# Kernel tuning notes

Hardware: AMD Instinct MI355X
Metric: run time of the kernel (lower is better)

The kernel has to match this reference:

```python
import jax, jax.numpy as jnp
import numpy as np

DT = 0.1  # fixed RK4 step size from the constructor

def setup_inputs() -> dict:
    key = jax.random.key(0)
    k1, k2, k3 = jax.random.split(key, 3)
    B, U, H = 65536, 128, 512
    x0 = jax.random.normal(k1, (B, U), dtype=jnp.float32)
    # small init so 20 unrolled RK4 steps stay numerically tame
    W1 = jax.random.normal(k2, (U, H), dtype=jnp.float32) * (0.5 / np.sqrt(U))
    b1 = jnp.zeros((H,), dtype=jnp.float32)
    W2 = jax.random.normal(k3, (H, U), dtype=jnp.float32) * (0.5 / np.sqrt(H))
    b2 = jnp.zeros((U,), dtype=jnp.float32)
    return {"x0": x0, "W1": W1, "b1": b1, "W2": W2, "b2": b2}

def _mlp(x, W1, b1, W2, b2):
    # vector field: Dense(512, relu) -> Dense(128); time-independent
    return jnp.maximum(x @ W1 + b1, 0.0) @ W2 + b2

def _rk4_integrate(x, n_steps, W1, b1, W2, b2):
    def step(x, _):
        k1 = _mlp(x, W1, b1, W2, b2)
        k2 = _mlp(x + 0.5 * DT * k1, W1, b1, W2, b2)
        k3 = _mlp(x + 0.5 * DT * k2, W1, b1, W2, b2)
        k4 = _mlp(x + DT * k3, W1, b1, W2, b2)
        return x + (DT / 6.0) * (k1 + 2.0 * k2 + 2.0 * k3 + k4), None
    x, _ = jax.lax.scan(step, x, None, length=n_steps)
    return x

def reference(x0, W1, b1, W2, b2):
    # phase 1: integrate t in [0, t1/2 = 1.0] -> 10 RK4 steps at dt=0.1
    x = _rk4_integrate(x0, 10, W1, b1, W2, b2)
    # phase 2: n=5 macro-steps of length (1.0 - 0.0)/5 = 0.2 -> 2 RK4 steps each
    def macro(x, _):
        x = _rk4_integrate(x, 2, W1, b1, W2, b2)
        return x, None
    x, _ = jax.lax.scan(macro, x, None, length=5)
    return x
```

## Files before the change

kernel.cpp:

```cpp
#include <hip/hip_runtime.h>
#include <stdint.h>


typedef _Float16 half8 __attribute__((ext_vector_type(8)));
typedef float f32x4 __attribute__((ext_vector_type(4)));
typedef __attribute__((address_space(3))) char lchar;
typedef __attribute__((address_space(1))) char gchar;

#define KSTR 136

static __device__ __forceinline__ void gload_lds16(const void* g, void* l) {
  __builtin_amdgcn_global_load_lds((const gchar*)g, (lchar*)l, 16, 0, 0);
}

static __device__ __forceinline__ unsigned short f2h(float x) {
  union { _Float16 h; unsigned short u; } cv;
  cv.h = (_Float16)x;
  return cv.u;
}

__global__ void pack_w(const float* __restrict__ W1, const float* __restrict__ W2,
                       unsigned short* __restrict__ w1p, unsigned short* __restrict__ w2p) {
  int id = blockIdx.x * 256 + threadIdx.x;
  int lane = id & 63, fid = (id >> 6) & 127;
  int g = lane >> 4, lm = lane & 15;
  if (id < 8192) {
    int c = fid >> 4, nt = (fid >> 2) & 3, ks = fid & 3;
    int n = c * 64 + nt * 16 + lm;
#pragma unroll
    for (int j = 0; j < 8; ++j) {
      int k = ks * 32 + g * 8 + j;
      w1p[fid * 512 + lane * 8 + j] = f2h(W1[k * 512 + n]);
    }
  } else {
    int c = fid >> 4, nt = (fid >> 1) & 7, ks = fid & 1;
    int u = nt * 16 + lm;
#pragma unroll
    for (int j = 0; j < 8; ++j) {
      int k = c * 64 + ks * 32 + g * 8 + j;
      w2p[fid * 512 + lane * 8 + j] = f2h(W2[k * 128 + u]);
    }
  }
}

__global__ __launch_bounds__(512, 2) void node_rk4(
    const float* __restrict__ x0, const float* __restrict__ b1,
    const float* __restrict__ b2, const unsigned short* __restrict__ w1p,
    const unsigned short* __restrict__ w2p, float* __restrict__ out) {
  __shared__ char Wbuf[2][32768];
  __shared__ unsigned short stg[8][32][KSTR];
  __shared__ float b1s[512];
  __shared__ float b2s[128];

  const int tid = threadIdx.x;
  const int w = tid >> 6, lane = tid & 63;
  const int g = lane >> 4, lm = lane & 15;
  unsigned short(*stage)[KSTR] = stg[w];

  b1s[tid] = b1[tid];
  if (tid < 128) b2s[tid] = b2[tid];

  const int rbase = blockIdx.x * 256 + w * 32;
  f32x4 xb[2][8], xa[2][8];
#pragma unroll
  for (int mt = 0; mt < 2; ++mt)
#pragma unroll
    for (int t = 0; t < 8; ++t) {
#pragma unroll
      for (int j = 0; j < 4; ++j)
        xb[mt][t][j] = x0[(rbase + mt * 16 + g * 4 + j) * 128 + t * 16 + lm];
      xa[mt][t] = xb[mt][t];
#pragma unroll
      for (int j = 0; j < 4; ++j)
        stage[mt * 16 + g * 4 + j][t * 16 + lm] = f2h(xb[mt][t][j]);
    }

  {
    const char* s1 = (const char*)w1p;
    const char* s2 = (const char*)w2p;
#pragma unroll
    for (int q = 0; q < 2; ++q) {
      int seg = w * 2 + q;
      gload_lds16(s1 + seg * 1024 + lane * 16, Wbuf[0] + seg * 1024);
      gload_lds16(s2 + seg * 1024 + lane * 16, Wbuf[0] + 16384 + seg * 1024);
    }
  }
  __syncthreads();

#pragma unroll 1
  for (int it = 0; it < 80; ++it) {
    const int s = it & 3;
    const float wgt = (s == 0 || s == 3) ? (0.1f / 6.0f) : (0.1f / 3.0f);
    const float alph = (s < 2) ? 0.05f : 0.1f;

    half8 A1[2][4];
#pragma unroll
    for (int mt = 0; mt < 2; ++mt)
#pragma unroll
      for (int ks = 0; ks < 4; ++ks)
        A1[mt][ks] = *(const half8*)&stage[mt * 16 + lm][ks * 32 + g * 8];

    f32x4 yacc[2][8];
#pragma unroll
    for (int mt = 0; mt < 2; ++mt)
#pragma unroll
      for (int t = 0; t < 8; ++t) yacc[mt][t] = f32x4{0.f, 0.f, 0.f, 0.f};

#pragma unroll
    for (int c = 0; c < 8; ++c) {
      {
        const int cn = (c + 1) & 7;
        char* buf = Wbuf[(c + 1) & 1];
        const char* s1 = (const char*)w1p + cn * 16384;
        const char* s2 = (const char*)w2p + cn * 16384;
#pragma unroll
        for (int q = 0; q < 2; ++q) {
          int seg = w * 2 + q;
          gload_lds16(s1 + seg * 1024 + lane * 16, buf + seg * 1024);
          gload_lds16(s2 + seg * 1024 + lane * 16, buf + 16384 + seg * 1024);
        }
      }
      const char* Wb = Wbuf[c & 1];

#pragma unroll
      for (int nt = 0; nt < 4; ++nt) {
        f32x4 h0 = {0.f, 0.f, 0.f, 0.f}, h1 = {0.f, 0.f, 0.f, 0.f};
#pragma unroll
        for (int ks = 0; ks < 4; ++ks) {
          half8 bf = *(const half8*)(Wb + (nt * 4 + ks) * 1024 + lane * 16);
          h0 = __builtin_amdgcn_mfma_f32_16x16x32_f16(A1[0][ks], bf, h0, 0, 0, 0);
          h1 = __builtin_amdgcn_mfma_f32_16x16x32_f16(A1[1][ks], bf, h1, 0, 0, 0);
        }
        float bb = b1s[c * 64 + nt * 16 + lm];
#pragma unroll
        for (int j = 0; j < 4; ++j) {
          stage[g * 4 + j][nt * 16 + lm] = f2h(fmaxf(h0[j] + bb, 0.f));
          stage[16 + g * 4 + j][nt * 16 + lm] = f2h(fmaxf(h1[j] + bb, 0.f));
        }
      }

      half8 A2[2][2];
#pragma unroll
      for (int mt = 0; mt < 2; ++mt)
#pragma unroll
        for (int k2 = 0; k2 < 2; ++k2)
          A2[mt][k2] = *(const half8*)&stage[mt * 16 + lm][k2 * 32 + g * 8];

#pragma unroll
      for (int nt = 0; nt < 8; ++nt)
#pragma unroll
        for (int k2 = 0; k2 < 2; ++k2) {
          half8 bf = *(const half8*)(Wb + 16384 + (nt * 2 + k2) * 1024 + lane * 16);
          yacc[0][nt] =
              __builtin_amdgcn_mfma_f32_16x16x32_f16(A2[0][k2], bf, yacc[0][nt], 0, 0, 0);
          yacc[1][nt] =
              __builtin_amdgcn_mfma_f32_16x16x32_f16(A2[1][k2], bf, yacc[1][nt], 0, 0, 0);
        }
      __syncthreads();
    }

#pragma unroll
    for (int mt = 0; mt < 2; ++mt)
#pragma unroll
      for (int t = 0; t < 8; ++t) {
        f32x4 k = yacc[mt][t];
        float bb = b2s[t * 16 + lm];
#pragma unroll
        for (int j = 0; j < 4; ++j) k[j] += bb;
        xa[mt][t] += wgt * k;
        f32x4 xi;
        if (s == 3) {
          xb[mt][t] = xa[mt][t];
          xi = xa[mt][t];
        } else {
          xi = xb[mt][t] + alph * k;
        }
#pragma unroll
        for (int j = 0; j < 4; ++j)
          stage[mt * 16 + g * 4 + j][t * 16 + lm] = f2h(xi[j]);
      }
  }

#pragma unroll
  for (int mt = 0; mt < 2; ++mt)
#pragma unroll
    for (int t = 0; t < 8; ++t)
#pragma unroll
      for (int j = 0; j < 4; ++j)
        out[(rbase + mt * 16 + g * 4 + j) * 128 + t * 16 + lm] = xb[mt][t][j];
}

extern "C" void kernel_launch(void* const* d_in, const int* in_sizes, int n_in,
                              void* d_out, int out_size, void* d_ws, size_t ws_size,
                              hipStream_t stream) {
  const float* x0 = (const float*)d_in[0];
  const float* W1 = (const float*)d_in[1];
  const float* b1 = (const float*)d_in[2];
  const float* W2 = (const float*)d_in[3];
  const float* b2 = (const float*)d_in[4];
  float* out = (float*)d_out;

  unsigned short* w1p = (unsigned short*)d_ws;
  unsigned short* w2p = w1p + 65536;

  pack_w<<<64, 256, 0, stream>>>(W1, W2, w1p, w2p);
  node_rk4<<<256, 512, 0, stream>>>(x0, b1, b2, w1p, w2p, out);
}
```

Baseline: 2.168 ms.

## Halve block size, interleave W1/W2 chunks, store RK4 base state in fp16

Blocks shrink from 512 to 256 threads (4 waves, 128 rows) and the grid doubles to 512. The hidden dimension is now streamed in 16 chunks of 32 columns, with W1 and W2 slices packed into a single interleaved 16KB buffer, which halves LDS use per block. The fp32 RK4 base state xb is replaced by an fp16 copy to free registers, with the aim of fitting more blocks per CU. The cost is twice as many per-chunk barriers and extra rounding of the intermediate stage inputs.

```diff
diff --git a/kernel.cpp b/kernel.cpp
--- a/kernel.cpp
+++ b/kernel.cpp
@@ -18,37 +18,43 @@
   cv.h = (_Float16)x;
   return cv.u;
 }
+static __device__ __forceinline__ float h2f(unsigned short u) {
+  union { unsigned short u; _Float16 h; } cv;
+  cv.u = u;
+  return (float)cv.h;
+}
 
 __global__ void pack_w(const float* __restrict__ W1, const float* __restrict__ W2,
-                       unsigned short* __restrict__ w1p, unsigned short* __restrict__ w2p) {
+                       unsigned short* __restrict__ wp) {
   int id = blockIdx.x * 256 + threadIdx.x;
-  int lane = id & 63, fid = (id >> 6) & 127;
+  int lane = id & 63, fid = (id >> 6) & 255;
   int g = lane >> 4, lm = lane & 15;
-  if (id < 8192) {
-    int c = fid >> 4, nt = (fid >> 2) & 3, ks = fid & 3;
-    int n = c * 64 + nt * 16 + lm;
+  int c = fid >> 4, f = fid & 15;
+  if (f < 8) {
+    int nt = f >> 2, ks = f & 3;
+    int n = c * 32 + nt * 16 + lm;
 #pragma unroll
     for (int j = 0; j < 8; ++j) {
       int k = ks * 32 + g * 8 + j;
-      w1p[fid * 512 + lane * 8 + j] = f2h(W1[k * 512 + n]);
+      wp[fid * 512 + lane * 8 + j] = f2h(W1[k * 512 + n]);
     }
   } else {
-    int c = fid >> 4, nt = (fid >> 1) & 7, ks = fid & 1;
+    int nt = f - 8;
     int u = nt * 16 + lm;
 #pragma unroll
     for (int j = 0; j < 8; ++j) {
-      int k = c * 64 + ks * 32 + g * 8 + j;
-      w2p[fid * 512 + lane * 8 + j] = f2h(W2[k * 128 + u]);
+      int k = c * 32 + g * 8 + j;
+      wp[fid * 512 + lane * 8 + j] = f2h(W2[k * 128 + u]);
     }
   }
 }
 
-__global__ __launch_bounds__(512, 2) void node_rk4(
+__global__ __launch_bounds__(256, 2) void node_rk4(
     const float* __restrict__ x0, const float* __restrict__ b1,
-    const float* __restrict__ b2, const unsigned short* __restrict__ w1p,
-    const unsigned short* __restrict__ w2p, float* __restrict__ out) {
-  __shared__ char Wbuf[2][32768];
-  __shared__ unsigned short stg[8][32][KSTR];
+    const float* __restrict__ b2, const unsigned short* __restrict__ wp,
+    float* __restrict__ out) {
+  __shared__ char Wbuf[2][16384];
+  __shared__ unsigned short stg[4][32][KSTR];
   __shared__ float b1s[512];
   __shared__ float b2s[128];
 
@@ -58,32 +64,33 @@
   unsigned short(*stage)[KSTR] = stg[w];
 
   b1s[tid] = b1[tid];
+  b1s[tid + 256] = b1[tid + 256];
   if (tid < 128) b2s[tid] = b2[tid];
 
-  const int rbase = blockIdx.x * 256 + w * 32;
-  f32x4 xb[2][8], xa[2][8];
+  const int rbase = blockIdx.x * 128 + w * 32;
+  f32x4 xa[2][8];
+  ushort4 xbh[2][8];
 #pragma unroll
   for (int mt = 0; mt < 2; ++mt)
 #pragma unroll
     for (int t = 0; t < 8; ++t) {
+      f32x4 v;
 #pragma unroll
       for (int j = 0; j < 4; ++j)
-        xb[mt][t][j] = x0[(rbase + mt * 16 + g * 4 + j) * 128 + t * 16 + lm];
-      xa[mt][t] = xb[mt][t];
+        v[j] = x0[(rbase + mt * 16 + g * 4 + j) * 128 + t * 16 + lm];
+      xa[mt][t] = v;
+      ushort4 hq;
+      hq.x = f2h(v[0]); hq.y = f2h(v[1]); hq.z = f2h(v[2]); hq.w = f2h(v[3]);
+      xbh[mt][t] = hq;
 #pragma unroll
       for (int j = 0; j < 4; ++j)
-        stage[mt * 16 + g * 4 + j][t * 16 + lm] = f2h(xb[mt][t][j]);
-    }
-
-  {
-    const char* s1 = (const char*)w1p;
-    const char* s2 = (const char*)w2p;
-#pragma unroll
-    for (int q = 0; q < 2; ++q) {
-      int seg = w * 2 + q;
-      gload_lds16(s1 + seg * 1024 + lane * 16, Wbuf[0] + seg * 1024);
-      gload_lds16(s2 + seg * 1024 + lane * 16, Wbuf[0] + 16384 + seg * 1024);
-    }
+        stage[mt * 16 + g * 4 + j][t * 16 + lm] = (&hq.x)[j];
+    }
+
+#pragma unroll
+  for (int q = 0; q < 4; ++q) {
+    int seg = w * 4 + q;
+    gload_lds16((const char*)wp + seg * 1024 + lane * 16, Wbuf[0] + seg * 1024);
   }
   __syncthreads();
 
@@ -107,23 +114,21 @@
       for (int t = 0; t < 8; ++t) yacc[mt][t] = f32x4{0.f, 0.f, 0.f, 0.f};
 
 #pragma unroll
-    for (int c = 0; c < 8; ++c) {
+    for (int c = 0; c < 16; ++c) {
       {
-        const int cn = (c + 1) & 7;
+        const int cn = (c + 1) & 15;
         char* buf = Wbuf[(c + 1) & 1];
-        const char* s1 = (const char*)w1p + cn * 16384;
-        const char* s2 = (const char*)w2p + cn * 16384;
-#pragma unroll
-        for (int q = 0; q < 2; ++q) {
-          int seg = w * 2 + q;
-          gload_lds16(s1 + seg * 1024 + lane * 16, buf + seg * 1024);
-          gload_lds16(s2 + seg * 1024 + lane * 16, buf + 16384 + seg * 1024);
+        const char* src = (const char*)wp + cn * 16384;
+#pragma unroll
+        for (int q = 0; q < 4; ++q) {
+          int seg = w * 4 + q;
+          gload_lds16(src + seg * 1024 + lane * 16, buf + seg * 1024);
         }
       }
       const char* Wb = Wbuf[c & 1];
 
 #pragma unroll
-      for (int nt = 0; nt < 4; ++nt) {
+      for (int nt = 0; nt < 2; ++nt) {
         f32x4 h0 = {0.f, 0.f, 0.f, 0.f}, h1 = {0.f, 0.f, 0.f, 0.f};
 #pragma unroll
         for (int ks = 0; ks < 4; ++ks) {
@@ -131,7 +136,7 @@
           h0 = __builtin_amdgcn_mfma_f32_16x16x32_f16(A1[0][ks], bf, h0, 0, 0, 0);
           h1 = __builtin_amdgcn_mfma_f32_16x16x32_f16(A1[1][ks], bf, h1, 0, 0, 0);
         }
-        float bb = b1s[c * 64 + nt * 16 + lm];
+        float bb = b1s[c * 32 + nt * 16 + lm];
 #pragma unroll
         for (int j = 0; j < 4; ++j) {
           stage[g * 4 + j][nt * 16 + lm] = f2h(fmaxf(h0[j] + bb, 0.f));
@@ -139,23 +144,16 @@
         }
       }
 
-      half8 A2[2][2];
+      half8 A2[2];
 #pragma unroll
       for (int mt = 0; mt < 2; ++mt)
-#pragma unroll
-        for (int k2 = 0; k2 < 2; ++k2)
-          A2[mt][k2] = *(const half8*)&stage[mt * 16 + lm][k2 * 32 + g * 8];
-
-#pragma unroll
-      for (int nt = 0; nt < 8; ++nt)
-#pragma unroll
-        for (int k2 = 0; k2 < 2; ++k2) {
-          half8 bf = *(const half8*)(Wb + 16384 + (nt * 2 + k2) * 1024 + lane * 16);
-          yacc[0][nt] =
-              __builtin_amdgcn_mfma_f32_16x16x32_f16(A2[0][k2], bf, yacc[0][nt], 0, 0, 0);
-          yacc[1][nt] =
-              __builtin_amdgcn_mfma_f32_16x16x32_f16(A2[1][k2], bf, yacc[1][nt], 0, 0, 0);
-        }
+        A2[mt] = *(const half8*)&stage[mt * 16 + lm][g * 8];
+#pragma unroll
+      for (int nt = 0; nt < 8; ++nt) {
+        half8 bf = *(const half8*)(Wb + 8192 + nt * 1024 + lane * 16);
+        yacc[0][nt] = __builtin_amdgcn_mfma_f32_16x16x32_f16(A2[0], bf, yacc[0][nt], 0, 0, 0);
+        yacc[1][nt] = __builtin_amdgcn_mfma_f32_16x16x32_f16(A2[1], bf, yacc[1][nt], 0, 0, 0);
+      }
       __syncthreads();
     }
 
@@ -168,16 +166,21 @@
 #pragma unroll
         for (int j = 0; j < 4; ++j) k[j] += bb;
         xa[mt][t] += wgt * k;
-        f32x4 xi;
+        ushort4 hq;
         if (s == 3) {
-          xb[mt][t] = xa[mt][t];
-          xi = xa[mt][t];
+          f32x4 v = xa[mt][t];
+          hq.x = f2h(v[0]); hq.y = f2h(v[1]); hq.z = f2h(v[2]); hq.w = f2h(v[3]);
+          xbh[mt][t] = hq;
         } else {
-          xi = xb[mt][t] + alph * k;
+          ushort4 xq = xbh[mt][t];
+          hq.x = f2h(h2f(xq.x) + alph * k[0]);
+          hq.y = f2h(h2f(xq.y) + alph * k[1]);
+          hq.z = f2h(h2f(xq.z) + alph * k[2]);
+          hq.w = f2h(h2f(xq.w) + alph * k[3]);
         }
 #pragma unroll
         for (int j = 0; j < 4; ++j)
-          stage[mt * 16 + g * 4 + j][t * 16 + lm] = f2h(xi[j]);
+          stage[mt * 16 + g * 4 + j][t * 16 + lm] = (&hq.x)[j];
       }
   }
 
@@ -187,7 +190,7 @@
     for (int t = 0; t < 8; ++t)
 #pragma unroll
       for (int j = 0; j < 4; ++j)
-        out[(rbase + mt * 16 + g * 4 + j) * 128 + t * 16 + lm] = xb[mt][t][j];
+        out[(rbase + mt * 16 + g * 4 + j) * 128 + t * 16 + lm] = xa[mt][t][j];
 }
 
 extern "C" void kernel_launch(void* const* d_in, const int* in_sizes, int n_in,
@@ -200,9 +203,8 @@
   const float* b2 = (const float*)d_in[4];
   float* out = (float*)d_out;
 
-  unsigned short* w1p = (unsigned short*)d_ws;
-  unsigned short* w2p = w1p + 65536;
-
-  pack_w<<<64, 256, 0, stream>>>(W1, W2, w1p, w2p);
-  node_rk4<<<256, 512, 0, stream>>>(x0, b1, b2, w1p, w2p, out);
-}
+  unsigned short* wp = (unsigned short*)d_ws;
+
+  pack_w<<<64, 256, 0, stream>>>(W1, W2, wp);
+  node_rk4<<<512, 256, 0, stream>>>(x0, b1, b2, wp, out);
+}
```

Result: slower. 3.506 ms (+61.7%).
